# Optimization experiments

Measured on AMD Instinct MI355X. Metric: run time of the kernel, lower is better.

## Reference

```python
import jax, jax.numpy as jnp
import numpy as np

B, S, DIM = 4, 1024, 4096
HQ, HKV, HD = 32, 8, 128
MAX_SEQ = 2048
START_POS = 1024
THETA = 10000.0


def _rope_tables(start, seqlen, head_dim, theta):
    inv = 1.0 / (theta ** (np.arange(0, head_dim, 2, dtype=np.float32) / head_dim))
    pos = np.arange(start, start + seqlen, dtype=np.float32)
    ang = np.outer(pos, inv)  # [S, HD/2]
    return jnp.asarray(np.cos(ang)), jnp.asarray(np.sin(ang))


def setup_inputs() -> dict:
    key = jax.random.key(0)
    ks = jax.random.split(key, 8)
    sc = 1.0 / np.sqrt(DIM)
    x = jax.random.normal(ks[0], (B, S, DIM), jnp.float32)
    wq = jax.random.normal(ks[1], (DIM, HQ * HD), jnp.float32) * sc
    wk = jax.random.normal(ks[2], (DIM, HKV * HD), jnp.float32) * sc
    wv = jax.random.normal(ks[3], (DIM, HKV * HD), jnp.float32) * sc
    wo = jax.random.normal(ks[4], (HQ * HD, DIM), jnp.float32) * sc
    cache_k = jax.random.normal(ks[5], (B, MAX_SEQ, HKV, HD), jnp.float32)
    cache_v = jax.random.normal(ks[6], (B, MAX_SEQ, HKV, HD), jnp.float32)
    cos, sin = _rope_tables(START_POS, S, HD, THETA)
    return {"x": x, "wq": wq, "wk": wk, "wv": wv, "wo": wo,
            "freqs_cos": cos, "freqs_sin": sin,
            "cache_k": cache_k, "cache_v": cache_v, "start_pos": START_POS}


def _apply_rope(t, cos, sin):
    # t: [B, S, H, HD]; cos/sin: [S, HD/2]
    b, s, h, d = t.shape
    tr = t.reshape(b, s, h, d // 2, 2)
    xr, xi = tr[..., 0], tr[..., 1]
    c = cos[None, :, None, :]
    sn = sin[None, :, None, :]
    outr = xr * c - xi * sn
    outi = xr * sn + xi * c
    return jnp.stack([outr, outi], axis=-1).reshape(b, s, h, d)


def reference(x, wq, wk, wv, wo, freqs_cos, freqs_sin, cache_k, cache_v, start_pos):
    b, s, _ = x.shape
    rep = HQ // HKV
    q = (x @ wq).reshape(b, s, HQ, HD)
    k = (x @ wk).reshape(b, s, HKV, HD)
    v = (x @ wv).reshape(b, s, HKV, HD)
    q = _apply_rope(q, freqs_cos, freqs_sin)
    k = _apply_rope(k, freqs_cos, freqs_sin)
    # write new K/V into the cache at start_pos (static int -> static slice)
    cache_k = cache_k.at[:, start_pos:start_pos + s].set(k)
    cache_v = cache_v.at[:, start_pos:start_pos + s].set(v)
    keys = cache_k[:, : start_pos + s]     # [B, KV, HKV, HD]
    values = cache_v[:, : start_pos + s]
    # GQA: group query heads with their KV head instead of materializing repeat_kv
    qg = q.reshape(b, s, HKV, rep, HD)
    scores = jnp.einsum('bqhrd,bkhd->bhrqk', qg, keys) / jnp.sqrt(
        jnp.asarray(HD, x.dtype))
    probs = jax.nn.softmax(scores, axis=-1).astype(x.dtype)
    out = jnp.einsum('bhrqk,bkhd->bqhrd', probs, values)
    out = out.reshape(b, s, HQ * HD)
    return out @ wo
```

## Files before the change

kernel.cpp:

```cpp
#include <hip/hip_runtime.h>

typedef _Float16 half_t;
typedef _Float16 half8 __attribute__((ext_vector_type(8)));
typedef _Float16 half4v __attribute__((ext_vector_type(4)));
typedef _Float16 half2v __attribute__((ext_vector_type(2)));
typedef float floatx4 __attribute__((ext_vector_type(4)));

#define TOK 4096
#define DIM 4096
#define S_LEN 1024
#define B_SZ 4
#define HQ_N 32
#define HKV_N 8
#define HD_N 128
#define L_KV 2048
#define NKV 1024
#define NQKV 6144
#define QK_SCALE 0.08838834764831845f
#define LOG2E 1.4426950408889634f

__device__ __forceinline__ void gload_lds16(const void* g, void* l) {
  __builtin_amdgcn_global_load_lds(
      (const __attribute__((address_space(1))) unsigned int*)g,
      (__attribute__((address_space(3))) unsigned int*)l, 16, 0, 0);
}

__device__ __forceinline__ float max3f(float a, float b, float c) {
  return fmaxf(fmaxf(a, b), c);
}

__global__ __launch_bounds__(256) void conv_x_kernel(const float* __restrict__ x,
                                                     half_t* __restrict__ xh) {
  int t = blockIdx.x * 256 + threadIdx.x;
  floatx4 v = *((const floatx4*)x + t);
  half4v o;
  o[0] = (half_t)v[0]; o[1] = (half_t)v[1]; o[2] = (half_t)v[2]; o[3] = (half_t)v[3];
  *((half4v*)xh + t) = o;
}

__global__ __launch_bounds__(256) void conv_transpose(const float* __restrict__ in,
                                                      half_t* __restrict__ out,
                                                      int K, int N) {
  __shared__ half_t T[64 * 65];
  const int tid = threadIdx.x;
  const int n0 = blockIdx.x * 64, k0 = blockIdx.y * 64;
  #pragma unroll
  for (int i = 0; i < 16; ++i) {
    int idx = i * 256 + tid;
    int r = idx >> 6, c = idx & 63;
    T[c * 65 + r] = (half_t)in[(size_t)(k0 + r) * N + n0 + c];
  }
  __syncthreads();
  #pragma unroll
  for (int i = 0; i < 16; ++i) {
    int idx = i * 256 + tid;
    int rn = idx >> 6, ck = idx & 63;
    out[(size_t)(n0 + rn) * K + k0 + ck] = T[rn * 65 + ck];
  }
}

template <typename OT>
__global__ __launch_bounds__(512) void gemm256(const half_t* __restrict__ A,
                                               const half_t* __restrict__ BT,
                                               OT* __restrict__ C,
                                               int M, int N, int K) {
  __shared__ __align__(16) char smem[131072];
  const int tid = threadIdx.x;
  const int lane = tid & 63, w = tid >> 6;
  const int g = lane >> 4, qr = lane & 15;
  const int wm = w >> 2, wn = w & 3;
  const int nbx = N >> 8;
  const int nwg = gridDim.x;
  const int cpx = nwg >> 3;
  const int bid = ((int)blockIdx.x & 7) * cpx + ((int)blockIdx.x >> 3);
  const int bx = bid % nbx, by = bid / nbx;
  const int m0 = by << 8, n0 = bx << 8;
  const int NT = K >> 6;

  const int ch0 = tid, ch1 = tid + 512;
  const int sr0 = ch0 >> 3, sc0 = (ch0 & 7) ^ (sr0 & 7);
  const int sr1 = ch1 >> 3, sc1 = (ch1 & 7) ^ (sr1 & 7);
  const size_t so0 = (size_t)sr0 * K + sc0 * 8;
  const size_t so1 = (size_t)sr1 * K + sc1 * 8;
  const int wb = (w * 64) * 16;
  const half_t* Ab = A + (size_t)m0 * K;
  const half_t* Bb = BT + (size_t)n0 * K;

#define G_STAGE(gsrc, ldst)                                   \
  do {                                                        \
    gload_lds16((gsrc) + so0, (char*)(ldst) + wb);            \
    gload_lds16((gsrc) + so1, (char*)(ldst) + wb + 8192);     \
  } while (0)

#define FRAG(base, row, kb) \
  (*(const half8*)((base) + ((((row) * 128) + (kb)) ^ (((row) & 7) << 4))))

  G_STAGE(Ab, smem);
  G_STAGE(Ab + (size_t)128 * K, smem + 16384);
  G_STAGE(Bb, smem + 65536);
  G_STAGE(Bb + (size_t)128 * K, smem + 81920);
  G_STAGE(Ab + 64, smem + 32768);
  G_STAGE(Bb + 64, smem + 98304);
  asm volatile("s_waitcnt vmcnt(4)" ::: "memory");
  __builtin_amdgcn_s_barrier();

  floatx4 acc[8][4] = {};
  half8 aF[4][2], bF0[2][2], bF1[2][2];

#define MFMA_Q(mh, nh, BF)                                                     \
  do {                                                                         \
    __builtin_amdgcn_s_setprio(1);                                             \
    _Pragma("unroll") for (int mf = 0; mf < 4; ++mf)                           \
    _Pragma("unroll") for (int nf = 0; nf < 2; ++nf)                           \
    _Pragma("unroll") for (int kk = 0; kk < 2; ++kk)                           \
      acc[(mh)*4 + mf][(nh)*2 + nf] = __builtin_amdgcn_mfma_f32_16x16x32_f16(  \
          aF[mf][kk], BF[nf][kk], acc[(mh)*4 + mf][(nh)*2 + nf], 0, 0, 0);     \
    __builtin_amdgcn_s_setprio(0);                                             \
  } while (0)

  for (int t = 0; t < NT; ++t) {
    const char* Ac = smem + ((t & 1) ? 32768 : 0);
    const char* Bc = smem + 65536 + ((t & 1) ? 32768 : 0);
    char* An = smem + ((t & 1) ? 0 : 32768);
    char* Bn = smem + 65536 + ((t & 1) ? 0 : 32768);
    const int t1 = (t + 1 < NT) ? t + 1 : NT - 1;
    const int t2 = (t + 2 < NT) ? t + 2 : NT - 1;
    #pragma unroll
    for (int mf = 0; mf < 4; ++mf)
      #pragma unroll
      for (int kk = 0; kk < 2; ++kk)
        aF[mf][kk] = FRAG(Ac, wm * 128 + mf * 16 + qr, kk * 64 + g * 16);
    #pragma unroll
    for (int nf = 0; nf < 2; ++nf)
      #pragma unroll
      for (int kk = 0; kk < 2; ++kk)
        bF0[nf][kk] = FRAG(Bc, wn * 64 + nf * 16 + qr, kk * 64 + g * 16);
    G_STAGE(Ab + (size_t)128 * K + t1 * 64, An + 16384);
    __builtin_amdgcn_s_barrier();
    asm volatile("s_waitcnt lgkmcnt(0)" ::: "memory");
    MFMA_Q(0, 0, bF0);
    __builtin_amdgcn_s_barrier();
    #pragma unroll
    for (int nf = 0; nf < 2; ++nf)
      #pragma unroll
      for (int kk = 0; kk < 2; ++kk)
        bF1[nf][kk] = FRAG(Bc, wn * 64 + 32 + nf * 16 + qr, kk * 64 + g * 16);
    G_STAGE(Bb + (size_t)128 * K + t1 * 64, Bn + 16384);
    __builtin_amdgcn_s_barrier();
    asm volatile("s_waitcnt lgkmcnt(0)" ::: "memory");
    MFMA_Q(0, 1, bF1);
    __builtin_amdgcn_s_barrier();
    #pragma unroll
    for (int mf = 0; mf < 4; ++mf)
      #pragma unroll
      for (int kk = 0; kk < 2; ++kk)
        aF[mf][kk] = FRAG(Ac, wm * 128 + 64 + mf * 16 + qr, kk * 64 + g * 16);
    __builtin_amdgcn_s_barrier();
    asm volatile("s_waitcnt lgkmcnt(0)" ::: "memory");
    MFMA_Q(1, 1, bF1);
    __builtin_amdgcn_s_barrier();
    G_STAGE(Ab + (size_t)t2 * 64, (char*)Ac);
    G_STAGE(Bb + (size_t)t2 * 64, (char*)Bc);
    __builtin_amdgcn_s_barrier();
    MFMA_Q(1, 0, bF0);
    asm volatile("s_waitcnt vmcnt(4)" ::: "memory");
    __builtin_amdgcn_s_barrier();
  }
  #pragma unroll
  for (int mh = 0; mh < 2; ++mh)
    #pragma unroll
    for (int mf = 0; mf < 4; ++mf) {
      const int rb = m0 + wm * 128 + mh * 64 + mf * 16 + g * 4;
      #pragma unroll
      for (int nh = 0; nh < 2; ++nh)
        #pragma unroll
        for (int nf = 0; nf < 2; ++nf) {
          const int col = n0 + wn * 64 + nh * 32 + nf * 16 + qr;
          floatx4 v = acc[mh * 4 + mf][nh * 2 + nf];
          #pragma unroll
          for (int r = 0; r < 4; ++r)
            C[(size_t)(rb + r) * N + col] = (OT)v[r];
        }
    }
#undef G_STAGE
#undef FRAG
#undef MFMA_Q
}

__global__ __launch_bounds__(256) void pack_q_kernel(const half_t* __restrict__ qkv,
                                                     const float* __restrict__ cosT,
                                                     const float* __restrict__ sinT,
                                                     half_t* __restrict__ qh) {
  int t = blockIdx.x * 256 + threadIdx.x;
  int j = t & 63;
  int hq = (t >> 6) & 31;
  int tok = t >> 11;
  int s = tok & 1023;
  int b = tok >> 10;
  const half_t* src = qkv + (size_t)tok * NQKV + hq * HD_N + 2 * j;
  float xr = (float)src[0], xi = (float)src[1];
  float c = cosT[s * 64 + j], sn = sinT[s * 64 + j];
  const float QS2 = QK_SCALE * LOG2E;
  half2v o;
  o[0] = (half_t)((xr * c - xi * sn) * QS2);
  o[1] = (half_t)((xr * sn + xi * c) * QS2);
  *(half2v*)(qh + ((size_t)((b * HQ_N + hq) * S_LEN + s)) * HD_N + 2 * j) = o;
}

__global__ __launch_bounds__(256) void pack_k_kernel(const half_t* __restrict__ qkv,
                                                     const float* __restrict__ cache_k,
                                                     const float* __restrict__ cosT,
                                                     const float* __restrict__ sinT,
                                                     half_t* __restrict__ kh) {
  int t = blockIdx.x * 256 + threadIdx.x;
  int j = t & 63;
  int h = (t >> 6) & 7;
  int pos = (t >> 9) & 2047;
  int b = t >> 20;
  float xr, xi;
  if (pos < 1024) {
    const float* src = cache_k + ((size_t)(b * L_KV + pos) * HKV_N + h) * HD_N + 2 * j;
    xr = src[0]; xi = src[1];
  } else {
    int s = pos - 1024;
    const half_t* src = qkv + (size_t)(b * S_LEN + s) * NQKV + DIM + h * HD_N + 2 * j;
    float r0 = (float)src[0], i0 = (float)src[1];
    float c = cosT[s * 64 + j], sn = sinT[s * 64 + j];
    xr = r0 * c - i0 * sn;
    xi = r0 * sn + i0 * c;
  }
  half2v o; o[0] = (half_t)xr; o[1] = (half_t)xi;
  *(half2v*)(kh + ((size_t)(b * HKV_N + h) * L_KV + pos) * HD_N + 2 * j) = o;
}

__global__ __launch_bounds__(256) void pack_vt_kernel(const half_t* __restrict__ qkv,
                                                      const float* __restrict__ cache_v,
                                                      half_t* __restrict__ vt) {
  __shared__ half_t T[128 * 129];
  const int tid = threadIdx.x;
  const int blk = blockIdx.x;
  const int pt = blk & 15;
  const int h = (blk >> 4) & 7;
  const int b = blk >> 7;
  const int p0 = pt * 128;
  #pragma unroll
  for (int i = 0; i < 64; ++i) {
    int idx = i * 256 + tid;
    int p = idx >> 7, d = idx & 127;
    int pos = p0 + p;
    float v;
    if (pos < 1024)
      v = cache_v[((size_t)(b * L_KV + pos) * HKV_N + h) * HD_N + d];
    else
      v = (float)qkv[(size_t)(b * S_LEN + (pos - 1024)) * NQKV + DIM + NKV + h * HD_N + d];
    T[d * 129 + p] = (half_t)v;
  }
  __syncthreads();
  #pragma unroll
  for (int i = 0; i < 64; ++i) {
    int idx = i * 256 + tid;
    int d = idx >> 7, p = idx & 127;
    vt[((size_t)(b * HKV_N + h) * HD_N + d) * L_KV + p0 + p] = T[d * 129 + p];
  }
}

__global__ __launch_bounds__(256) void attn_kernel(const half_t* __restrict__ qh,
                                                   const half_t* __restrict__ kh,
                                                   const half_t* __restrict__ vt,
                                                   half_t* __restrict__ ah) {
  __shared__ __align__(16) char smem[74752];
  const int tid = threadIdx.x;
  const int lane = tid & 63, w = tid >> 6;
  const int g = lane >> 4, qr = lane & 15;
  const int qt = blockIdx.x, hq = blockIdx.y, b = blockIdx.z;
  const int hkv = hq >> 2;
  const half_t* qbase =
      qh + ((size_t)((b * HQ_N + hq) * S_LEN) + qt * 64 + w * 16 + qr) * HD_N;
  half8 qf[4];
  #pragma unroll
  for (int c = 0; c < 4; ++c) qf[c] = *(const half8*)(qbase + g * 8 + c * 32);
  floatx4 acc[8] = {};
  float m_run = -1e30f, l_run = 0.f;
  const half_t* kg = kh + (size_t)(b * HKV_N + hkv) * L_KV * HD_N;
  const half_t* vg = vt + (size_t)(b * HKV_N + hkv) * HD_N * L_KV;

  const int sw = (qr & 7) << 4;
  const char* kqkP[4];
  #pragma unroll
  for (int c = 0; c < 4; ++c) kqkP[c] = smem + qr * 256 + ((g * 16 + c * 64) ^ sw);
  const char* vP[2];
  #pragma unroll
  for (int kc = 0; kc < 2; ++kc)
    vP[kc] = smem + 32768 + qr * 128 + ((kc * 64 + g * 16) ^ sw);
  char* pwP = smem + 65536 + w * 2304 + qr * 144 + g * 8;
  const char* prP = smem + 65536 + w * 2304 + qr * 144 + g * 16;

  const int r0 = tid >> 4;
  const int c8k = (tid & 15) ^ (r0 & 7);
  const half_t* kp[4];
  #pragma unroll
  for (int j = 0; j < 4; ++j) kp[j] = kg + (size_t)(r0 + 16 * j) * HD_N + c8k * 8;
  const int d0 = tid >> 3;
  const int p8v = (tid & 7) ^ (d0 & 7);
  const half_t* vp[4];
  #pragma unroll
  for (int j = 0; j < 4; ++j) vp[j] = vg + (size_t)(d0 + 32 * j) * L_KV + p8v * 8;
  const int ldsb = (tid & 192) * 16;

#define ISSUE_STAGE(NKB)                                                     \
  do {                                                                       \
    _Pragma("unroll") for (int j2 = 0; j2 < 4; ++j2)                         \
      gload_lds16(kp[j2], smem + (NKB) + ldsb + j2 * 4096);                  \
    _Pragma("unroll") for (int j2 = 0; j2 < 4; ++j2)                         \
      gload_lds16(vp[j2], smem + 32768 + (NKB) + ldsb + j2 * 4096);          \
    _Pragma("unroll") for (int j2 = 0; j2 < 4; ++j2) {                       \
      kp[j2] += 8192; vp[j2] += 64;                                          \
    }                                                                        \
  } while (0)

#define COMPUTE(KB)                                                            \
  do {                                                                         \
    float sc[16];                                                              \
    __builtin_amdgcn_s_setprio(1);                                             \
    _Pragma("unroll") for (int ts = 0; ts < 4; ++ts) {                         \
      floatx4 tq = {0.f, 0.f, 0.f, 0.f};                                       \
      _Pragma("unroll") for (int c = 0; c < 4; ++c)                            \
        tq = __builtin_amdgcn_mfma_f32_16x16x32_f16(                           \
            *(const half8*)(kqkP[c] + (KB) + ts * 4096), qf[c], tq, 0, 0, 0);  \
      sc[ts*4+0]=tq[0]; sc[ts*4+1]=tq[1]; sc[ts*4+2]=tq[2]; sc[ts*4+3]=tq[3];  \
    }                                                                          \
    __builtin_amdgcn_s_setprio(0);                                             \
    float pmax = fmaxf(                                                        \
        max3f(max3f(sc[0], sc[1], sc[2]), max3f(sc[3], sc[4], sc[5]),          \
              max3f(sc[6], sc[7], sc[8])),                                     \
        max3f(max3f(sc[9], sc[10], sc[11]), max3f(sc[12], sc[13], sc[14]),     \
              sc[15]));                                                        \
    pmax = fmaxf(pmax, __shfl_xor(pmax, 16, 64));                              \
    pmax = fmaxf(pmax, __shfl_xor(pmax, 32, 64));                              \
    const bool skip = __all(pmax - m_run <= 8.f);                              \
    const float mnew = skip ? m_run : fmaxf(m_run, pmax);                      \
    float rs = 0.f;                                                            \
    _Pragma("unroll") for (int j = 0; j < 16; ++j) {                           \
      float p;                                                                 \
      asm("v_exp_f32 %0, %1" : "=v"(p) : "v"(sc[j] - mnew));                   \
      sc[j] = p; rs += p;                                                      \
    }                                                                          \
    rs += __shfl_xor(rs, 16, 64);                                              \
    rs += __shfl_xor(rs, 32, 64);                                              \
    if (skip) {                                                                \
      l_run += rs;                                                             \
    } else {                                                                   \
      float scl;                                                               \
      asm("v_exp_f32 %0, %1" : "=v"(scl) : "v"(m_run - mnew));                 \
      l_run = l_run * scl + rs;                                                \
      float f0 = __shfl(scl, g * 4 + 0, 64), f1 = __shfl(scl, g * 4 + 1, 64);  \
      float f2 = __shfl(scl, g * 4 + 2, 64), f3 = __shfl(scl, g * 4 + 3, 64);  \
      _Pragma("unroll") for (int n = 0; n < 8; ++n) {                          \
        acc[n][0] *= f0; acc[n][1] *= f1; acc[n][2] *= f2; acc[n][3] *= f3;    \
      }                                                                        \
      m_run = mnew;                                                            \
    }                                                                          \
    _Pragma("unroll") for (int ts = 0; ts < 4; ++ts) {                         \
      half2v lo = __builtin_bit_cast(                                          \
          half2v, __builtin_amdgcn_cvt_pkrtz(sc[ts * 4 + 0], sc[ts * 4 + 1])); \
      half2v hi = __builtin_bit_cast(                                          \
          half2v, __builtin_amdgcn_cvt_pkrtz(sc[ts * 4 + 2], sc[ts * 4 + 3])); \
      *(half4v*)(pwP + ts * 32) = __builtin_shufflevector(lo, hi, 0, 1, 2, 3); \
    }                                                                          \
    __builtin_amdgcn_s_setprio(1);                                             \
    _Pragma("unroll") for (int kc = 0; kc < 2; ++kc) {                         \
      half8 pf = *(const half8*)(prP + kc * 64);                               \
      _Pragma("unroll") for (int n = 0; n < 8; ++n)                            \
        acc[n] = __builtin_amdgcn_mfma_f32_16x16x32_f16(                       \
            pf, *(const half8*)(vP[kc] + (KB) + n * 2048), acc[n], 0, 0, 0);   \
    }                                                                          \
    __builtin_amdgcn_s_setprio(0);                                             \
  } while (0)

#define ENDBAR                                          \
  do {                                                  \
    asm volatile("s_waitcnt vmcnt(0)" ::: "memory");    \
    __builtin_amdgcn_s_barrier();                       \
  } while (0)

  ISSUE_STAGE(0);
  ENDBAR;
  for (int it = 0; it < 15; ++it) {
    ISSUE_STAGE(16384); COMPUTE(0);     ENDBAR;
    ISSUE_STAGE(0);     COMPUTE(16384); ENDBAR;
  }
  ISSUE_STAGE(16384); COMPUTE(0); ENDBAR;
  COMPUTE(16384);

  float il0 = 1.f / __shfl(l_run, g * 4 + 0, 64);
  float il1 = 1.f / __shfl(l_run, g * 4 + 1, 64);
  float il2 = 1.f / __shfl(l_run, g * 4 + 2, 64);
  float il3 = 1.f / __shfl(l_run, g * 4 + 3, 64);
  const int tokb = b * S_LEN + qt * 64 + w * 16 + g * 4;
  #pragma unroll
  for (int n = 0; n < 8; ++n) {
    const int col = hq * HD_N + n * 16 + qr;
    ah[(size_t)(tokb + 0) * DIM + col] = (half_t)(acc[n][0] * il0);
    ah[(size_t)(tokb + 1) * DIM + col] = (half_t)(acc[n][1] * il1);
    ah[(size_t)(tokb + 2) * DIM + col] = (half_t)(acc[n][2] * il2);
    ah[(size_t)(tokb + 3) * DIM + col] = (half_t)(acc[n][3] * il3);
  }
#undef ISSUE_STAGE
#undef COMPUTE
#undef ENDBAR
}

extern "C" void kernel_launch(void* const* d_in, const int* in_sizes, int n_in,
                              void* d_out, int out_size, void* d_ws, size_t ws_size,
                              hipStream_t stream) {
  (void)in_sizes; (void)n_in; (void)out_size; (void)ws_size;
  const float* x = (const float*)d_in[0];
  const float* wq = (const float*)d_in[1];
  const float* wk = (const float*)d_in[2];
  const float* wv = (const float*)d_in[3];
  const float* wo = (const float*)d_in[4];
  const float* fc = (const float*)d_in[5];
  const float* fs = (const float*)d_in[6];
  const float* ck = (const float*)d_in[7];
  const float* cv = (const float*)d_in[8];

  char* ws = (char*)d_ws;
  size_t off = 0;
  auto alloc = [&](size_t bytes) {
    char* p = ws + off;
    off += (bytes + 255) & ~(size_t)255;
    return p;
  };
  half_t* xh     = (half_t*)alloc((size_t)TOK * DIM * 2);
  half_t* W      = (half_t*)alloc((size_t)NQKV * DIM * 2);
  half_t* qkvf16 = (half_t*)alloc((size_t)TOK * NQKV * 2);
  half_t* kh     = (half_t*)alloc((size_t)B_SZ * HKV_N * L_KV * HD_N * 2);
  half_t* vth    = (half_t*)alloc((size_t)B_SZ * HKV_N * HD_N * L_KV * 2);
  half_t* qh     = xh;
  half_t* ah     = W;
  half_t* woT    = qkvf16;

  conv_x_kernel<<<dim3(TOK * DIM / 4 / 256), dim3(256), 0, stream>>>(x, xh);
  conv_transpose<<<dim3(DIM / 64, DIM / 64), dim3(256), 0, stream>>>(wq, W, DIM, DIM);
  conv_transpose<<<dim3(NKV / 64, DIM / 64), dim3(256), 0, stream>>>(wk, W + (size_t)DIM * DIM, DIM, NKV);
  conv_transpose<<<dim3(NKV / 64, DIM / 64), dim3(256), 0, stream>>>(wv, W + (size_t)(DIM + NKV) * DIM, DIM, NKV);
  gemm256<half_t><<<dim3((TOK / 256) * (NQKV / 256)), dim3(512), 0, stream>>>(xh, W, qkvf16, TOK, NQKV, DIM);
  pack_q_kernel<<<dim3(B_SZ * S_LEN * HQ_N * 64 / 256), dim3(256), 0, stream>>>(qkvf16, fc, fs, qh);
  pack_k_kernel<<<dim3(B_SZ * L_KV * HKV_N * 64 / 256), dim3(256), 0, stream>>>(qkvf16, ck, fc, fs, kh);
  pack_vt_kernel<<<dim3(B_SZ * HKV_N * (L_KV / 128)), dim3(256), 0, stream>>>(qkvf16, cv, vth);
  attn_kernel<<<dim3(S_LEN / 64, HQ_N, B_SZ), dim3(256), 0, stream>>>(qh, kh, vth, ah);
  conv_transpose<<<dim3(DIM / 64, DIM / 64), dim3(256), 0, stream>>>(wo, woT, DIM, DIM);
  gemm256<float><<<dim3((TOK / 256) * (DIM / 256)), dim3(512), 0, stream>>>(ah, woT, (float*)d_out, TOK, DIM, DIM);
}
```

Measured before the change: 701.7 us.

## Process two query tiles per attention block to reuse staged K/V

```diff
diff --git a/kernel.cpp b/kernel.cpp
--- a/kernel.cpp
+++ b/kernel.cpp
@@ -264,10 +264,10 @@
   }
 }
 
-__global__ __launch_bounds__(256) void attn_kernel(const half_t* __restrict__ qh,
-                                                   const half_t* __restrict__ kh,
-                                                   const half_t* __restrict__ vt,
-                                                   half_t* __restrict__ ah) {
+__global__ __launch_bounds__(256, 2) void attn_kernel(const half_t* __restrict__ qh,
+                                                      const half_t* __restrict__ kh,
+                                                      const half_t* __restrict__ vt,
+                                                      half_t* __restrict__ ah) {
   __shared__ __align__(16) char smem[74752];
   const int tid = threadIdx.x;
   const int lane = tid & 63, w = tid >> 6;
@@ -275,12 +275,15 @@
   const int qt = blockIdx.x, hq = blockIdx.y, b = blockIdx.z;
   const int hkv = hq >> 2;
   const half_t* qbase =
-      qh + ((size_t)((b * HQ_N + hq) * S_LEN) + qt * 64 + w * 16 + qr) * HD_N;
-  half8 qf[4];
-  #pragma unroll
-  for (int c = 0; c < 4; ++c) qf[c] = *(const half8*)(qbase + g * 8 + c * 32);
-  floatx4 acc[8] = {};
-  float m_run = -1e30f, l_run = 0.f;
+      qh + ((size_t)((b * HQ_N + hq) * S_LEN) + qt * 128 + w * 16 + qr) * HD_N;
+  half8 qfA[4], qfB[4];
+  #pragma unroll
+  for (int c = 0; c < 4; ++c) {
+    qfA[c] = *(const half8*)(qbase + g * 8 + c * 32);
+    qfB[c] = *(const half8*)(qbase + (size_t)64 * HD_N + g * 8 + c * 32);
+  }
+  floatx4 accA[8] = {}, accB[8] = {};
+  float mA = -1e30f, lA = 0.f, mB = -1e30f, lB = 0.f;
   const half_t* kg = kh + (size_t)(b * HKV_N + hkv) * L_KV * HD_N;
   const half_t* vg = vt + (size_t)(b * HKV_N + hkv) * HD_N * L_KV;
 
@@ -318,63 +321,75 @@
     }                                                                        \
   } while (0)
 
-#define COMPUTE(KB)                                                            \
+#define QKT(QF, SC, KB)                                                        \
   do {                                                                         \
-    float sc[16];                                                              \
     __builtin_amdgcn_s_setprio(1);                                             \
     _Pragma("unroll") for (int ts = 0; ts < 4; ++ts) {                         \
       floatx4 tq = {0.f, 0.f, 0.f, 0.f};                                       \
       _Pragma("unroll") for (int c = 0; c < 4; ++c)                            \
         tq = __builtin_amdgcn_mfma_f32_16x16x32_f16(                           \
-            *(const half8*)(kqkP[c] + (KB) + ts * 4096), qf[c], tq, 0, 0, 0);  \
-      sc[ts*4+0]=tq[0]; sc[ts*4+1]=tq[1]; sc[ts*4+2]=tq[2]; sc[ts*4+3]=tq[3];  \
+            *(const half8*)(kqkP[c] + (KB) + ts * 4096), QF[c], tq, 0, 0, 0);  \
+      SC[ts*4+0]=tq[0]; SC[ts*4+1]=tq[1]; SC[ts*4+2]=tq[2]; SC[ts*4+3]=tq[3];  \
     }                                                                          \
     __builtin_amdgcn_s_setprio(0);                                             \
+  } while (0)
+
+#define SOFTPV(SC, ACC, MR, LR, KB)                                            \
+  do {                                                                         \
     float pmax = fmaxf(                                                        \
-        max3f(max3f(sc[0], sc[1], sc[2]), max3f(sc[3], sc[4], sc[5]),          \
-              max3f(sc[6], sc[7], sc[8])),                                     \
-        max3f(max3f(sc[9], sc[10], sc[11]), max3f(sc[12], sc[13], sc[14]),     \
-              sc[15]));                                                        \
+        max3f(max3f(SC[0], SC[1], SC[2]), max3f(SC[3], SC[4], SC[5]),          \
+              max3f(SC[6], SC[7], SC[8])),                                     \
+        max3f(max3f(SC[9], SC[10], SC[11]), max3f(SC[12], SC[13], SC[14]),     \
+              SC[15]));                                                        \
     pmax = fmaxf(pmax, __shfl_xor(pmax, 16, 64));                              \
     pmax = fmaxf(pmax, __shfl_xor(pmax, 32, 64));                              \
-    const bool skip = __all(pmax - m_run <= 8.f);                              \
-    const float mnew = skip ? m_run : fmaxf(m_run, pmax);                      \
+    const bool skip = __all(pmax - MR <= 8.f);                                 \
+    const float mnew = skip ? MR : fmaxf(MR, pmax);                            \
     float rs = 0.f;                                                            \
     _Pragma("unroll") for (int j = 0; j < 16; ++j) {                           \
       float p;                                                                 \
-      asm("v_exp_f32 %0, %1" : "=v"(p) : "v"(sc[j] - mnew));                   \
-      sc[j] = p; rs += p;                                                      \
+      asm("v_exp_f32 %0, %1" : "=v"(p) : "v"(SC[j] - mnew));                   \
+      SC[j] = p; rs += p;                                                      \
     }                                                                          \
     rs += __shfl_xor(rs, 16, 64);                                              \
     rs += __shfl_xor(rs, 32, 64);                                              \
     if (skip) {                                                                \
-      l_run += rs;                                                             \
+      LR += rs;                                                                \
     } else {                                                                   \
       float scl;                                                               \
-      asm("v_exp_f32 %0, %1" : "=v"(scl) : "v"(m_run - mnew));                 \
-      l_run = l_run * scl + rs;                                                \
+      asm("v_exp_f32 %0, %1" : "=v"(scl) : "v"(MR - mnew));                    \
+      LR = LR * scl + rs;                                                      \
       float f0 = __shfl(scl, g * 4 + 0, 64), f1 = __shfl(scl, g * 4 + 1, 64);  \
       float f2 = __shfl(scl, g * 4 + 2, 64), f3 = __shfl(scl, g * 4 + 3, 64);  \
       _Pragma("unroll") for (int n = 0; n < 8; ++n) {                          \
-        acc[n][0] *= f0; acc[n][1] *= f1; acc[n][2] *= f2; acc[n][3] *= f3;    \
+        ACC[n][0] *= f0; ACC[n][1] *= f1; ACC[n][2] *= f2; ACC[n][3] *= f3;    \
       }                                                                        \
-      m_run = mnew;                                                            \
+      MR = mnew;                                                               \
     }                                                                          \
     _Pragma("unroll") for (int ts = 0; ts < 4; ++ts) {                         \
       half2v lo = __builtin_bit_cast(                                          \
-          half2v, __builtin_amdgcn_cvt_pkrtz(sc[ts * 4 + 0], sc[ts * 4 + 1])); \
+          half2v, __builtin_amdgcn_cvt_pkrtz(SC[ts * 4 + 0], SC[ts * 4 + 1])); \
       half2v hi = __builtin_bit_cast(                                          \
-          half2v, __builtin_amdgcn_cvt_pkrtz(sc[ts * 4 + 2], sc[ts * 4 + 3])); \
+          half2v, __builtin_amdgcn_cvt_pkrtz(SC[ts * 4 + 2], SC[ts * 4 + 3])); \
       *(half4v*)(pwP + ts * 32) = __builtin_shufflevector(lo, hi, 0, 1, 2, 3); \
     }                                                                          \
     __builtin_amdgcn_s_setprio(1);                                             \
     _Pragma("unroll") for (int kc = 0; kc < 2; ++kc) {                         \
       half8 pf = *(const half8*)(prP + kc * 64);                               \
       _Pragma("unroll") for (int n = 0; n < 8; ++n)                            \
-        acc[n] = __builtin_amdgcn_mfma_f32_16x16x32_f16(                       \
-            pf, *(const half8*)(vP[kc] + (KB) + n * 2048), acc[n], 0, 0, 0);   \
+        ACC[n] = __builtin_amdgcn_mfma_f32_16x16x32_f16(                       \
+            pf, *(const half8*)(vP[kc] + (KB) + n * 2048), ACC[n], 0, 0, 0);   \
     }                                                                          \
     __builtin_amdgcn_s_setprio(0);                                             \
+  } while (0)
+
+#define COMPUTE2(KB)                       \
+  do {                                     \
+    float scA[16], scB[16];                \
+    QKT(qfA, scA, KB);                     \
+    QKT(qfB, scB, KB);                     \
+    SOFTPV(scA, accA, mA, lA, KB);         \
+    SOFTPV(scB, accB, mB, lB, KB);         \
   } while (0)
 
 #define ENDBAR                                          \
@@ -386,28 +401,36 @@
   ISSUE_STAGE(0);
   ENDBAR;
   for (int it = 0; it < 15; ++it) {
-    ISSUE_STAGE(16384); COMPUTE(0);     ENDBAR;
-    ISSUE_STAGE(0);     COMPUTE(16384); ENDBAR;
-  }
-  ISSUE_STAGE(16384); COMPUTE(0); ENDBAR;
-  COMPUTE(16384);
-
-  float il0 = 1.f / __shfl(l_run, g * 4 + 0, 64);
-  float il1 = 1.f / __shfl(l_run, g * 4 + 1, 64);
-  float il2 = 1.f / __shfl(l_run, g * 4 + 2, 64);
-  float il3 = 1.f / __shfl(l_run, g * 4 + 3, 64);
-  const int tokb = b * S_LEN + qt * 64 + w * 16 + g * 4;
-  #pragma unroll
-  for (int n = 0; n < 8; ++n) {
-    const int col = hq * HD_N + n * 16 + qr;
-    ah[(size_t)(tokb + 0) * DIM + col] = (half_t)(acc[n][0] * il0);
-    ah[(size_t)(tokb + 1) * DIM + col] = (half_t)(acc[n][1] * il1);
-    ah[(size_t)(tokb + 2) * DIM + col] = (half_t)(acc[n][2] * il2);
-    ah[(size_t)(tokb + 3) * DIM + col] = (half_t)(acc[n][3] * il3);
-  }
+    ISSUE_STAGE(16384); COMPUTE2(0);     ENDBAR;
+    ISSUE_STAGE(0);     COMPUTE2(16384); ENDBAR;
+  }
+  ISSUE_STAGE(16384); COMPUTE2(0); ENDBAR;
+  COMPUTE2(16384);
+
+#define WRITE_OUT(ACC, LR, SOFF)                                            \
+  do {                                                                      \
+    float il0 = 1.f / __shfl(LR, g * 4 + 0, 64);                            \
+    float il1 = 1.f / __shfl(LR, g * 4 + 1, 64);                            \
+    float il2 = 1.f / __shfl(LR, g * 4 + 2, 64);                            \
+    float il3 = 1.f / __shfl(LR, g * 4 + 3, 64);                            \
+    const int tokb = b * S_LEN + qt * 128 + (SOFF) + w * 16 + g * 4;        \
+    _Pragma("unroll") for (int n = 0; n < 8; ++n) {                         \
+      const int col = hq * HD_N + n * 16 + qr;                              \
+      ah[(size_t)(tokb + 0) * DIM + col] = (half_t)(ACC[n][0] * il0);       \
+      ah[(size_t)(tokb + 1) * DIM + col] = (half_t)(ACC[n][1] * il1);       \
+      ah[(size_t)(tokb + 2) * DIM + col] = (half_t)(ACC[n][2] * il2);       \
+      ah[(size_t)(tokb + 3) * DIM + col] = (half_t)(ACC[n][3] * il3);       \
+    }                                                                       \
+  } while (0)
+
+  WRITE_OUT(accA, lA, 0);
+  WRITE_OUT(accB, lB, 64);
 #undef ISSUE_STAGE
-#undef COMPUTE
+#undef QKT
+#undef SOFTPV
+#undef COMPUTE2
 #undef ENDBAR
+#undef WRITE_OUT
 }
 
 extern "C" void kernel_launch(void* const* d_in, const int* in_sizes, int n_in,
@@ -448,7 +471,7 @@
   pack_q_kernel<<<dim3(B_SZ * S_LEN * HQ_N * 64 / 256), dim3(256), 0, stream>>>(qkvf16, fc, fs, qh);
   pack_k_kernel<<<dim3(B_SZ * L_KV * HKV_N * 64 / 256), dim3(256), 0, stream>>>(qkvf16, ck, fc, fs, kh);
   pack_vt_kernel<<<dim3(B_SZ * HKV_N * (L_KV / 128)), dim3(256), 0, stream>>>(qkvf16, cv, vth);
-  attn_kernel<<<dim3(S_LEN / 64, HQ_N, B_SZ), dim3(256), 0, stream>>>(qh, kh, vth, ah);
+  attn_kernel<<<dim3(S_LEN / 128, HQ_N, B_SZ), dim3(256), 0, stream>>>(qh, kh, vth, ah);
   conv_transpose<<<dim3(DIM / 64, DIM / 64), dim3(256), 0, stream>>>(wo, woT, DIM, DIM);
   gemm256<float><<<dim3((TOK / 256) * (DIM / 256)), dim3(512), 0, stream>>>(ah, woT, (float*)d_out, TOK, DIM, DIM);
 }
```

New measurement: 665.8 us. 5.1% less time.
